# Kernel optimization log

Measured on AMD Instinct MI355X. Metric: run time of the kernel, lower is better.

The kernel has to match this reference:

```python
import jax, jax.numpy as jnp
import numpy as np

D = 256; H = 8; HD = D // H; NK = 32; NLAYERS = 4; FF = 4 * D
B = 8; M = 768; N = 128; LT = 64; T = M + N + LT
SCALE = 1.0 / float(np.sqrt(HD))


def layer_norm(x, s, b):
    mu = x.mean(-1, keepdims=True)
    var = ((x - mu) ** 2).mean(-1, keepdims=True)
    return (x - mu) * jax.lax.rsqrt(var + 1e-5) * s + b


def sine_embed(pos, d):
    # MTR gen_sineembed_for_position: half dims for y, half for x, interleaved sin/cos
    half = d // 2
    dim_t = jnp.power(10000.0, 2.0 * (jnp.arange(half) // 2).astype(jnp.float32) / half)
    scale = 2.0 * np.pi
    def inter(e):
        return jnp.stack([jnp.sin(e[:, 0::2]), jnp.cos(e[:, 1::2])], -1).reshape(e.shape[0], -1)
    ex = pos[:, 0:1] * scale / dim_t
    ey = pos[:, 1:2] * scale / dim_t
    return jnp.concatenate([inter(ey), inter(ex)], -1)


def setup_inputs() -> dict:
    key = jax.random.key(0)
    ks = jax.random.split(key, 24)
    s = 0.02
    inp = {
        'map_token': jax.random.normal(ks[0], (B, M, D), jnp.float32),
        'agent_token': jax.random.normal(ks[1], (B, N, D), jnp.float32),
        'light_token': jax.random.normal(ks[2], (B, LT, D), jnp.float32),
        'map_position': jax.random.uniform(ks[3], (B, M, 2), jnp.float32) * 100.0,
        'agent_position': jax.random.uniform(ks[4], (B, N, 2), jnp.float32) * 100.0,
        'light_position': jax.random.uniform(ks[5], (B, LT, 2), jnp.float32) * 100.0,
        'map_valid_mask': jnp.ones((B, M), bool),
        'agent_valid_mask': jnp.ones((B, N), bool),
        'light_valid_mask': jnp.ones((B, LT), bool),
        'Wq': jax.random.normal(ks[6], (NLAYERS, D, D), jnp.float32) * s,
        'bq': jnp.zeros((NLAYERS, D), jnp.float32),
        'Wk': jax.random.normal(ks[7], (NLAYERS, D, D), jnp.float32) * s,
        'bk': jnp.zeros((NLAYERS, D), jnp.float32),
        'Wv': jax.random.normal(ks[8], (NLAYERS, D, D), jnp.float32) * s,
        'bv': jnp.zeros((NLAYERS, D), jnp.float32),
        'Wo': jax.random.normal(ks[9], (NLAYERS, D, D), jnp.float32) * s,
        'bo': jnp.zeros((NLAYERS, D), jnp.float32),
        'W1': jax.random.normal(ks[10], (NLAYERS, D, FF), jnp.float32) * s,
        'b1': jnp.zeros((NLAYERS, FF), jnp.float32),
        'W2': jax.random.normal(ks[11], (NLAYERS, FF, D), jnp.float32) * s,
        'b2': jnp.zeros((NLAYERS, D), jnp.float32),
        'ln1_s': jnp.ones((NLAYERS, D), jnp.float32),
        'ln1_b': jnp.zeros((NLAYERS, D), jnp.float32),
        'ln2_s': jnp.ones((NLAYERS, D), jnp.float32),
        'ln2_b': jnp.zeros((NLAYERS, D), jnp.float32),
    }
    return inp


def reference(map_token, agent_token, light_token, map_position, agent_position, light_position,
              map_valid_mask, agent_valid_mask, light_valid_mask,
              Wq, bq, Wk, bk, Wv, bv, Wo, bo, W1, b1, W2, b2, ln1_s, ln1_b, ln2_s, ln2_b):
    x = jnp.concatenate([map_token, agent_token, light_token], 1)             # [B,T,D]
    pos = jnp.concatenate([map_position, agent_position, light_position], 1)[..., :2]  # [B,T,2]
    # all tokens valid -> masked compaction is a static reshape
    xs = x.reshape(B * T, D)
    ps = pos.reshape(B * T, 2)
    # KNN within each scene (includes self, like knn_batch_mlogk on same set)
    d2 = jnp.sum((pos[:, :, None, :] - pos[:, None, :, :]) ** 2, -1)          # [B,T,T]
    _, idx = jax.lax.top_k(-d2, NK)                                            # [B,T,NK] local indices
    idx = (idx + (jnp.arange(B) * T)[:, None, None]).reshape(B * T, NK)        # global flat indices
    pe = sine_embed(ps, D)                                                     # [B*T,D]
    out = xs
    for l in range(NLAYERS):
        qk = out + pe
        q = (qk @ Wq[l] + bq[l]).reshape(-1, H, HD)
        k = (qk @ Wk[l] + bk[l]).reshape(-1, H, HD)
        v = (out @ Wv[l] + bv[l]).reshape(-1, H, HD)
        kn = k[idx]                                                            # [BT,NK,H,HD] gather
        vn = v[idx]
        att = jax.nn.softmax(jnp.einsum('nhd,nkhd->nhk', q, kn) * SCALE, axis=-1)
        a = jnp.einsum('nhk,nkhd->nhd', att, vn).reshape(-1, D) @ Wo[l] + bo[l]
        out = layer_norm(out + a, ln1_s[l], ln1_b[l])
        ff = jax.nn.relu(out @ W1[l] + b1[l]) @ W2[l] + b2[l]
        out = layer_norm(out + ff, ln2_s[l], ln2_b[l])
    full = out.reshape(B, T, D)
    return full[:, :M], full[:, M:M + N], full[:, M + N:]
```

## Files before the change

### kernel.cpp

```cpp
#include <hip/hip_runtime.h>
#include <math.h>

#define BB 8
#define MTOK 768
#define NTOK 128
#define LTOK 64
#define TT 960
#define BT 7680
#define DD 256
#define HH 8
#define HD 32
#define KNN 32
#define FFD 1024
#define NLAYERS 4
#define SCALE_ATT 0.17677669529663687f

typedef __attribute__((ext_vector_type(8))) short bfrag_t;
typedef __attribute__((ext_vector_type(4))) float accfrag_t;

__device__ __forceinline__ float b2f(unsigned short u) {
  union { unsigned int i; float f; } c; c.i = ((unsigned int)u) << 16; return c.f;
}
__device__ __forceinline__ unsigned short f2b(float f) {
  union { float f; unsigned int i; } c; c.f = f;
  return (unsigned short)((c.i + 0x7fffu + ((c.i >> 16) & 1u)) >> 16);
}
__device__ __forceinline__ float load_elem(const void* p, size_t i, int f) {
  return f ? b2f(((const unsigned short*)p)[i]) : ((const float*)p)[i];
}
__device__ __forceinline__ size_t pk_addr(int row, int col, int nks) {
  return ((size_t)((row >> 4) * nks + (col >> 5)) << 9)
       + (size_t)(((((col >> 3) & 3) << 4) + (row & 15)) * 8 + (col & 7));
}
__device__ __forceinline__ int swiz_tok(int blk) { return (blk & 7) * TT + (blk >> 3); }

#define FB_BQ 0
#define FB_BK 1024
#define FB_BV 2048
#define FB_BO 3072
#define FB_B1 4096
#define FB_B2 8192
#define FB_LN1S 9216
#define FB_LN1B 10240
#define FB_LN2S 11264
#define FB_LN2B 12288
#define FB_TOTAL 13312
struct ParamSrc { const void* p[13]; };
__global__ __launch_bounds__(256)
void conv_misc_kernel(ParamSrc ps, const void* tok, int* flagout,
                      float* __restrict__ dst, float* __restrict__ posf) {
  __shared__ int cnt;
  if (threadIdx.x == 0) cnt = 0;
  __syncthreads();
  const unsigned short* u = (const unsigned short*)tok;
  int ok = 0;
  for (int i = threadIdx.x; i < 1024; i += 256) {
    int e = (u[i] >> 7) & 0xFF;
    if (e >= 100 && e <= 140) ok++;
  }
  atomicAdd(&cnt, ok);
  __syncthreads();
  int f = (cnt >= 922) ? 1 : 0;
  if (blockIdx.x == 0 && threadIdx.x == 0) *flagout = f;
  if (blockIdx.x < BB) {
    int b = blockIdx.x;
    for (int t = threadIdx.x; t < TT * 2; t += 256) {
      int tok2 = t >> 1, c = t & 1;
      const void* p; size_t idx;
      if (tok2 < MTOK)             { p = ps.p[10]; idx = (size_t)(b * MTOK + tok2) * 2 + c; }
      else if (tok2 < MTOK + NTOK) { p = ps.p[11]; idx = (size_t)(b * NTOK + tok2 - MTOK) * 2 + c; }
      else                         { p = ps.p[12]; idx = (size_t)(b * LTOK + tok2 - MTOK - NTOK) * 2 + c; }
      posf[((size_t)b * TT + tok2) * 2 + c] = load_elem(p, idx, f);
    }
    return;
  }
  int i = (blockIdx.x - BB) * 256 + threadIdx.x;
  if (i >= FB_TOTAL) return;
  int src; size_t off;
  if (i < 4096)      { src = i >> 10;              off = i & 1023; }
  else if (i < 8192) { src = 4;                    off = i - 4096; }
  else               { src = 5 + ((i - 8192) >> 10); off = (i - 8192) & 1023; }
  dst[i] = load_elem(ps.p[src], off, f);
}

__device__ __forceinline__ unsigned long long shfl_xor_u64(unsigned long long v, int m) {
  unsigned lo = (unsigned)v, hi = (unsigned)(v >> 32);
  lo = (unsigned)__shfl_xor((int)lo, m);
  hi = (unsigned)__shfl_xor((int)hi, m);
  return ((unsigned long long)hi << 32) | (unsigned long long)lo;
}
__device__ __forceinline__ unsigned long long shfl_u64(unsigned long long v, int srcLane) {
  unsigned lo = (unsigned)v, hi = (unsigned)(v >> 32);
  lo = (unsigned)__shfl((int)lo, srcLane);
  hi = (unsigned)__shfl((int)hi, srcLane);
  return ((unsigned long long)hi << 32) | (unsigned long long)lo;
}
__device__ __forceinline__ unsigned long long bitonic64(unsigned long long key, int lane) {
#pragma unroll
  for (int kk = 2; kk <= 64; kk <<= 1) {
#pragma unroll
    for (int j = kk >> 1; j > 0; j >>= 1) {
      unsigned long long other = shfl_xor_u64(key, j);
      bool small_ = (lane & j) == 0;
      bool dir = (lane & kk) == 0;
      bool keep = ((key < other) == (small_ == dir));
      key = keep ? key : other;
    }
  }
  return key;
}

struct PackSrc { const void* s[6]; };
__global__ __launch_bounds__(256)
void mega_kernel(PackSrc w, const void* mt, const void* at, const void* lt,
                 const float* __restrict__ posf, const int* __restrict__ flag,
                 unsigned short* __restrict__ Wqkvpk, unsigned short* __restrict__ Wopk,
                 unsigned short* __restrict__ W1pk, unsigned short* __restrict__ W2pk,
                 unsigned short* __restrict__ pe_b, float* __restrict__ out_f,
                 unsigned short* __restrict__ pk1, unsigned short* __restrict__ qkpk,
                 int* __restrict__ idx_out) {
  __shared__ float sx[TT], sy[TT];
  __shared__ unsigned long long cbuf[4][64];
  int bid = blockIdx.x;
  if (bid < 12288) {
    int f = *flag;
    int id = bid * 256 + threadIdx.x;
    if (id < 786432) {
      int layer = id / 196608, rest = id % 196608;
      int sel = rest >> 16, e = rest & 65535;
      int k = e >> 8, col = e & 255;
      const void* src = w.s[sel];
      size_t si = (size_t)layer * 65536 + e;
      Wqkvpk[(size_t)layer * 196608 + (size_t)sel * 65536 + pk_addr(col, k, 8)] =
          f ? ((const unsigned short*)src)[si] : f2b(((const float*)src)[si]);
    } else if (id < 1048576) {
      int off = id - 786432, layer = off >> 16, e = off & 65535;
      int k = e >> 8, col = e & 255;
      size_t si = (size_t)layer * 65536 + e;
      Wopk[(size_t)layer * 65536 + pk_addr(col, k, 8)] =
          f ? ((const unsigned short*)w.s[3])[si] : f2b(((const float*)w.s[3])[si]);
    } else if (id < 2097152) {
      int off = id - 1048576, layer = off >> 18, e = off & 262143;
      int k = e >> 10, col = e & 1023;
      size_t si = (size_t)layer * 262144 + e;
      W1pk[(size_t)layer * 262144 + pk_addr(col, k, 8)] =
          f ? ((const unsigned short*)w.s[4])[si] : f2b(((const float*)w.s[4])[si]);
    } else {
      int off = id - 2097152, layer = off >> 18, e = off & 262143;
      int k = e >> 8, col = e & 255;
      size_t si = (size_t)layer * 262144 + e;
      W2pk[(size_t)layer * 262144 + pk_addr(col, k, 32)] =
          f ? ((const unsigned short*)w.s[5])[si] : f2b(((const float*)w.s[5])[si]);
    }
    return;
  }
  if (bid < 19968) {
    int n = swiz_tok(bid - 12288), d = threadIdx.x;
    int b = n / TT, t = n - b * TT;
    int f = *flag;
    const void* src; size_t si;
    if (t < MTOK)              { src = mt; si = (size_t)(b * MTOK + t) * DD + d; }
    else if (t < MTOK + NTOK)  { src = at; si = (size_t)(b * NTOK + (t - MTOK)) * DD + d; }
    else                       { src = lt; si = (size_t)(b * LTOK + (t - MTOK - NTOK)) * DD + d; }
    float x = load_elem(src, si, f);
    float px = posf[((size_t)b * TT + t) * 2 + 0];
    float py = posf[((size_t)b * TT + t) * 2 + 1];
    float coord = (d < 128) ? py : px;
    int j = d & 127;
    float expo = (float)(2 * (j >> 1)) / 128.0f;
    float dim_t = powf(10000.0f, expo);
    float e = coord * 6.283185307179586f / dim_t;
    float p = (j & 1) ? cosf(e) : sinf(e);
    size_t o = (size_t)n * DD + d;
    pe_b[o] = f2b(p);
    out_f[o] = x;
    size_t pa = pk_addr(n, d, 8);
    pk1[pa] = f2b(x);
    qkpk[pa] = f2b(x + p);
    return;
  }
  int kb = bid - 19968;
  int b = kb & 7;
  int qbase = (kb >> 3) * 4;
  for (int t = threadIdx.x; t < TT; t += 256) {
    sx[t] = posf[((size_t)b * TT + t) * 2 + 0];
    sy[t] = posf[((size_t)b * TT + t) * 2 + 1];
  }
  __syncthreads();
  int wave = threadIdx.x >> 6, lane = threadIdx.x & 63;
  int t = qbase + wave;
  float qx = sx[t], qy = sy[t];

  unsigned long long k[15];
#pragma unroll
  for (int c = 0; c < 15; c++) {
    int j = c * 64 + lane;
    float dx = qx - sx[j], dy = qy - sy[j];
    float d2 = __fadd_rn(__fmul_rn(dx, dx), __fmul_rn(dy, dy));
    k[c] = ((unsigned long long)__float_as_uint(d2) << 32) | (unsigned)j;
  }
  unsigned long long lm = k[0];
#pragma unroll
  for (int c = 1; c < 15; c++) lm = (k[c] < lm) ? k[c] : lm;

  unsigned long long sm = bitonic64(lm, lane);
  unsigned long long thr = shfl_u64(sm, 31);

  int c_l = 0;
#pragma unroll
  for (int c = 0; c < 15; c++) c_l += (k[c] <= thr) ? 1 : 0;
  int inc = c_l;
#pragma unroll
  for (int o = 1; o < 64; o <<= 1) {
    int tt = __shfl_up(inc, o);
    inc += (lane >= o) ? tt : 0;
  }
  int total = __shfl(inc, 63);
  int pos = inc - c_l;

  if (total <= 64) {
    unsigned long long* wb = cbuf[wave];
#pragma unroll
    for (int c = 0; c < 15; c++) {
      if (k[c] <= thr) { wb[pos] = k[c]; pos++; }
    }
    unsigned long long cand = (lane < total) ? wb[lane] : ~0ull;
    cand = bitonic64(cand, lane);
    if (lane < KNN)
      idx_out[((size_t)(b * TT + t)) * KNN + lane] = b * TT + (int)(cand & 0xFFFFFFFFu);
  } else {
    unsigned res = 0;
    for (int i = 0; i < KNN; i++) {
      unsigned long long m = k[0];
#pragma unroll
      for (int c = 1; c < 15; c++) m = (k[c] < m) ? k[c] : m;
#pragma unroll
      for (int o = 32; o > 0; o >>= 1) {
        unsigned long long om = shfl_xor_u64(m, o);
        m = (om < m) ? om : m;
      }
      if (lane == i) res = (unsigned)(m & 0xFFFFFFFFu);
      int owner = (int)(m & 63u), ch = (int)(((unsigned)(m & 0xFFFFFFFFu)) >> 6);
      if (lane == owner) {
#pragma unroll
        for (int c = 0; c < 15; c++) if (c == ch) k[c] = ~0ull;
      }
    }
    if (lane < KNN)
      idx_out[((size_t)(b * TT + t)) * KNN + lane] = b * TT + (int)res;
  }
}

template<int NKS, int NT>
__device__ __forceinline__ void wavegemm(const unsigned short* __restrict__ Apk,
                                         const unsigned short* __restrict__ Bpk,
                                         int rb, int cb0, accfrag_t (&acc)[NT]) {
  const int lane = threadIdx.x & 63;
  accfrag_t z = {0.f, 0.f, 0.f, 0.f};
#pragma unroll
  for (int nt = 0; nt < NT; nt++) acc[nt] = z;
  const unsigned short* ap = Apk + ((size_t)rb * NKS * 512 + lane * 8);
  const unsigned short* bp = Bpk + ((size_t)cb0 * NKS * 512 + lane * 8);
#pragma unroll 4
  for (int ks = 0; ks < NKS; ks++) {
    bfrag_t a = *(const bfrag_t*)(ap + ks * 512);
#pragma unroll
    for (int nt = 0; nt < NT; nt++) {
      bfrag_t b = *(const bfrag_t*)(bp + (size_t)(nt * NKS + ks) * 512);
      acc[nt] = __builtin_amdgcn_mfma_f32_16x16x32_bf16(a, b, acc[nt], 0, 0, 0);
    }
  }
}

__global__ __launch_bounds__(256)
void qkv_kernel(const unsigned short* __restrict__ qkpk,
                const unsigned short* __restrict__ outpk,
                const unsigned short* __restrict__ Wl,
                const float* __restrict__ pb, int l,
                unsigned short* __restrict__ QKV) {
  int scene = blockIdx.x & 7, r = blockIdx.x >> 3;
  int rbg = r % 15, cgall = r / 15;
  int wave = threadIdx.x >> 6, lane = threadIdx.x & 63;
  int rb = scene * 60 + rbg * 4 + wave;
  int sel = cgall >> 2, cg = cgall & 3;
  const unsigned short* A = (sel < 2) ? qkpk : outpk;
  const unsigned short* B = Wl + sel * 65536;
  const float* bias = pb + sel * 1024 + l * 256;
  accfrag_t acc[4];
  wavegemm<8,4>(A, B, rb, cg * 4, acc);
  int l16 = lane & 15, lq = lane >> 4;
  unsigned short* C = QKV + (size_t)sel * BT * DD;
#pragma unroll
  for (int nt = 0; nt < 4; nt++) {
    int col = cg * 64 + nt * 16 + l16;
    float bv = bias[col];
#pragma unroll
    for (int r4 = 0; r4 < 4; r4++) {
      int row = rb * 16 + lq * 4 + r4;
      C[(size_t)row * DD + col] = f2b(acc[nt][r4] + bv);
    }
  }
}

__global__ __launch_bounds__(256)
void attn_kernel(const unsigned short* __restrict__ QKV,
                 const int* __restrict__ idx,
                 unsigned short* __restrict__ attnpk) {
  __shared__ unsigned short kn[KNN][DD + 8];
  __shared__ unsigned short vn[KNN][DD + 8];
  __shared__ float qs[DD];
  __shared__ float att[HH][KNN];
  __shared__ int nb[KNN];
  const unsigned short* Q = QKV;
  const unsigned short* K = QKV + (size_t)BT * DD;
  const unsigned short* V = QKV + 2 * (size_t)BT * DD;
  int n = swiz_tok(blockIdx.x), tid = threadIdx.x;
  if (tid < KNN) nb[tid] = idx[n * KNN + tid];
  qs[tid] = b2f(Q[(size_t)n * DD + tid]);
  __syncthreads();
#pragma unroll
  for (int p = 0; p < 4; p++) {
    int e = p * 256 + tid;
    int r = e >> 5, c8 = (e & 31) * 8;
    int srow = nb[r];
    *(uint4*)(&kn[r][c8]) = *(const uint4*)(K + (size_t)srow * DD + c8);
    *(uint4*)(&vn[r][c8]) = *(const uint4*)(V + (size_t)srow * DD + c8);
  }
  __syncthreads();
  int h = tid >> 5, kk = tid & 31;
  float dot = 0.0f;
#pragma unroll
  for (int d = 0; d < HD; d++) dot += qs[h * HD + d] * b2f(kn[kk][h * HD + d]);
  float sc = dot * SCALE_ATT;
  float mx = sc;
#pragma unroll
  for (int o = 16; o > 0; o >>= 1) mx = fmaxf(mx, __shfl_xor(mx, o, 32));
  float ex = expf(sc - mx);
  float sm = ex;
#pragma unroll
  for (int o = 16; o > 0; o >>= 1) sm += __shfl_xor(sm, o, 32);
  att[h][kk] = ex / sm;
  __syncthreads();
  int d = kk;
  float oacc = 0.0f;
#pragma unroll
  for (int k2 = 0; k2 < KNN; k2++) oacc += att[h][k2] * b2f(vn[k2][h * HD + d]);
  attnpk[pk_addr(n, tid, 8)] = f2b(oacc);
}

template<bool LAST>
__global__ __launch_bounds__(256)
void ffn_block_kernel(const unsigned short* __restrict__ attnpk,
                      const unsigned short* __restrict__ Wo,
                      const unsigned short* __restrict__ W1,
                      const unsigned short* __restrict__ W2,
                      const unsigned short* __restrict__ Wn,
                      const float* __restrict__ bo,
                      const float* __restrict__ b1,
                      const float* __restrict__ b2,
                      const float* __restrict__ pb, int ln,
                      float* __restrict__ yf,
                      const unsigned short* __restrict__ pe_b,
                      const float* __restrict__ g1, const float* __restrict__ t1,
                      const float* __restrict__ g2, const float* __restrict__ t2,
                      unsigned short* __restrict__ QKV,
                      void* __restrict__ dout, const int* __restrict__ flag) {
  __shared__ unsigned short xls[8 * 512];
  __shared__ unsigned short hls[32 * 512];
  __shared__ float ps1[4][16], ps2[4][16];
  int scene = blockIdx.x & 7, rbs = blockIdx.x >> 3;
  int wave = threadIdx.x >> 6, lane = threadIdx.x & 63;
  int rb = scene * 60 + rbs;
  int l16 = lane & 15, lq = lane >> 4;

  float resv[4][4];
#pragma unroll
  for (int nt = 0; nt < 4; nt++) {
    int col = wave * 64 + nt * 16 + l16;
#pragma unroll
    for (int r4 = 0; r4 < 4; r4++) {
      int row = rb * 16 + lq * 4 + r4;
      resv[nt][r4] = yf[(size_t)row * DD + col];
    }
  }

  accfrag_t acc[4];
  wavegemm<8,4>(attnpk, Wo, rb, wave * 4, acc);
  float y[4][4];
  float s[4] = {0.f, 0.f, 0.f, 0.f}, s2[4] = {0.f, 0.f, 0.f, 0.f};
#pragma unroll
  for (int nt = 0; nt < 4; nt++) {
    int col = wave * 64 + nt * 16 + l16;
    float bv = bo[col];
#pragma unroll
    for (int r4 = 0; r4 < 4; r4++) {
      float x = acc[nt][r4] + bv + resv[nt][r4];
      y[nt][r4] = x; s[r4] += x; s2[r4] += x * x;
    }
  }
#pragma unroll
  for (int o = 1; o < 16; o <<= 1) {
#pragma unroll
    for (int r4 = 0; r4 < 4; r4++) { s[r4] += __shfl_xor(s[r4], o); s2[r4] += __shfl_xor(s2[r4], o); }
  }
  if (l16 == 0) {
#pragma unroll
    for (int r4 = 0; r4 < 4; r4++) { ps1[wave][lq * 4 + r4] = s[r4]; ps2[wave][lq * 4 + r4] = s2[r4]; }
  }
  __syncthreads();
#pragma unroll
  for (int r4 = 0; r4 < 4; r4++) {
    int r16 = lq * 4 + r4;
    float ts  = ps1[0][r16] + ps1[1][r16] + ps1[2][r16] + ps1[3][r16];
    float ts2 = ps2[0][r16] + ps2[1][r16] + ps2[2][r16] + ps2[3][r16];
    float mu = ts * (1.0f / 256.0f);
    float var = ts2 * (1.0f / 256.0f) - mu * mu;
    float rstd = 1.0f / sqrtf(fmaxf(var, 0.f) + 1e-5f);
#pragma unroll
    for (int nt = 0; nt < 4; nt++) {
      int col = wave * 64 + nt * 16 + l16;
      float v = (y[nt][r4] - mu) * rstd * g1[col] + t1[col];
      y[nt][r4] = v;
      xls[pk_addr(r16, col, 8)] = f2b(v);
    }
  }
  __syncthreads();

#pragma unroll
  for (int i = 0; i < 4; i++) {
    int cg = wave * 4 + i;
    accfrag_t a2[4];
    wavegemm<8,4>(xls, W1, 0, cg * 4, a2);
#pragma unroll
    for (int nt = 0; nt < 4; nt++) {
      int col = cg * 64 + nt * 16 + l16;
      float bv = b1[col];
#pragma unroll
      for (int r4 = 0; r4 < 4; r4++)
        hls[pk_addr(lq * 4 + r4, col, 32)] = f2b(fmaxf(a2[nt][r4] + bv, 0.0f));
    }
  }
  __syncthreads();

  accfrag_t a3[4];
  wavegemm<32,4>(hls, W2, 0, wave * 4, a3);
  float v2[4][4];
  float s3[4] = {0.f, 0.f, 0.f, 0.f}, s4[4] = {0.f, 0.f, 0.f, 0.f};
#pragma unroll
  for (int nt = 0; nt < 4; nt++) {
    int col = wave * 64 + nt * 16 + l16;
    float bv = b2[col];
#pragma unroll
    for (int r4 = 0; r4 < 4; r4++) {
      float x = a3[nt][r4] + bv + y[nt][r4];
      v2[nt][r4] = x; s3[r4] += x; s4[r4] += x * x;
    }
  }
#pragma unroll
  for (int o = 1; o < 16; o <<= 1) {
#pragma unroll
    for (int r4 = 0; r4 < 4; r4++) { s3[r4] += __shfl_xor(s3[r4], o); s4[r4] += __shfl_xor(s4[r4], o); }
  }
  if (l16 == 0) {
#pragma unroll
    for (int r4 = 0; r4 < 4; r4++) { ps1[wave][lq * 4 + r4] = s3[r4]; ps2[wave][lq * 4 + r4] = s4[r4]; }
  }
  __syncthreads();
  unsigned short* qkls = hls;
  int fl = LAST ? *flag : 0;
#pragma unroll
  for (int r4 = 0; r4 < 4; r4++) {
    int r16 = lq * 4 + r4;
    float ts  = ps1[0][r16] + ps1[1][r16] + ps1[2][r16] + ps1[3][r16];
    float ts2 = ps2[0][r16] + ps2[1][r16] + ps2[2][r16] + ps2[3][r16];
    float mu = ts * (1.0f / 256.0f);
    float var = ts2 * (1.0f / 256.0f) - mu * mu;
    float rstd = 1.0f / sqrtf(fmaxf(var, 0.f) + 1e-5f);
#pragma unroll
    for (int nt = 0; nt < 4; nt++) {
      int col = wave * 64 + nt * 16 + l16;
      float yv = (v2[nt][r4] - mu) * rstd * g2[col] + t2[col];
      int row = rb * 16 + r16;
      if (!LAST) {
        yf[(size_t)row * DD + col] = yv;
        float q = yv + b2f(pe_b[(size_t)row * DD + col]);
        xls[pk_addr(r16, col, 8)] = f2b(yv);
        qkls[pk_addr(r16, col, 8)] = f2b(q);
      } else {
        int t = rbs * 16 + r16;
        size_t o;
        if (t < MTOK)             o = (size_t)(scene * MTOK + t) * DD + col;
        else if (t < MTOK + NTOK) o = (size_t)BB * MTOK * DD + (size_t)(scene * NTOK + (t - MTOK)) * DD + col;
        else                      o = (size_t)BB * MTOK * DD + (size_t)BB * NTOK * DD
                                    + (size_t)(scene * LTOK + (t - MTOK - NTOK)) * DD + col;
        if (fl) ((unsigned short*)dout)[o] = f2b(yv);
        else    ((float*)dout)[o] = yv;
      }
    }
  }

  if (!LAST) {
    __syncthreads();
#pragma unroll
    for (int i = 0; i < 3; i++) {
      int cgall = wave * 3 + i;
      int sel = cgall >> 2, cg = cgall & 3;
      const unsigned short* A = (sel < 2) ? qkls : xls;
      accfrag_t a4[4];
      wavegemm<8,4>(A, Wn + sel * 65536, 0, cg * 4, a4);
      const float* bias = pb + sel * 1024 + ln * 256;
      unsigned short* C = QKV + (size_t)sel * BT * DD;
#pragma unroll
      for (int nt = 0; nt < 4; nt++) {
        int col = cg * 64 + nt * 16 + l16;
        float bv = bias[col];
#pragma unroll
        for (int r4 = 0; r4 < 4; r4++) {
          int row = rb * 16 + lq * 4 + r4;
          C[(size_t)row * DD + col] = f2b(a4[nt][r4] + bv);
        }
      }
    }
  }
}

extern "C" void kernel_launch(void* const* d_in, const int* in_sizes, int n_in,
                              void* d_out, int out_size, void* d_ws, size_t ws_size,
                              hipStream_t stream) {
  const void* map_tok   = d_in[0];
  const void* agent_tok = d_in[1];
  const void* light_tok = d_in[2];
  const void* map_pos   = d_in[3];
  const void* agent_pos = d_in[4];
  const void* light_pos = d_in[5];
  const void* Wq  = d_in[9];
  const void* bq  = d_in[10];
  const void* Wk  = d_in[11];
  const void* bk  = d_in[12];
  const void* Wv  = d_in[13];
  const void* bv  = d_in[14];
  const void* Wo  = d_in[15];
  const void* bo  = d_in[16];
  const void* W1  = d_in[17];
  const void* b1  = d_in[18];
  const void* W2  = d_in[19];
  const void* b2  = d_in[20];
  const void* ln1s = d_in[21];
  const void* ln1b = d_in[22];
  const void* ln2s = d_in[23];
  const void* ln2b = d_in[24];

  size_t off = 0;
  char* base = (char*)d_ws;
  auto take = [&](size_t bytes) { char* p = base + off; off += (bytes + 255) & ~(size_t)255; return (void*)p; };
  int*   flag  = (int*)take(256);
  float* posf  = (float*)take((size_t)BT * 2 * 4);
  float* pbuf  = (float*)take((size_t)FB_TOTAL * 4);
  unsigned short* pe_b = (unsigned short*)take((size_t)BT * DD * 2);
  float* out_f = (float*)take((size_t)BT * DD * 4);
  unsigned short* pk1  = (unsigned short*)take((size_t)BT * DD * 2);
  unsigned short* qkpk = (unsigned short*)take((size_t)BT * DD * 2);
  unsigned short* QKV  = (unsigned short*)take((size_t)3 * BT * DD * 2);
  unsigned short* attnpk = (unsigned short*)take((size_t)BT * DD * 2);
  int* idxb = (int*)take((size_t)BT * KNN * 4);
  unsigned short* Wqkvpk = (unsigned short*)take((size_t)NLAYERS * 3 * DD * DD * 2);
  unsigned short* Wopk   = (unsigned short*)take((size_t)NLAYERS * DD * DD * 2);
  unsigned short* W1pk   = (unsigned short*)take((size_t)NLAYERS * DD * FFD * 2);
  unsigned short* W2pk   = (unsigned short*)take((size_t)NLAYERS * DD * FFD * 2);

  ParamSrc ps; ps.p[0]=bq; ps.p[1]=bk; ps.p[2]=bv; ps.p[3]=bo; ps.p[4]=b1;
  ps.p[5]=b2; ps.p[6]=ln1s; ps.p[7]=ln1b; ps.p[8]=ln2s; ps.p[9]=ln2b;
  ps.p[10]=map_pos; ps.p[11]=agent_pos; ps.p[12]=light_pos;
  conv_misc_kernel<<<BB + (FB_TOTAL + 255) / 256, 256, 0, stream>>>(ps, map_tok, flag, pbuf, posf);

  PackSrc pw; pw.s[0]=Wq; pw.s[1]=Wk; pw.s[2]=Wv; pw.s[3]=Wo; pw.s[4]=W1; pw.s[5]=W2;
  mega_kernel<<<21888, 256, 0, stream>>>(pw, map_tok, agent_tok, light_tok, posf, flag,
                                         Wqkvpk, Wopk, W1pk, W2pk,
                                         pe_b, out_f, pk1, qkpk, idxb);

  qkv_kernel<<<1440, 256, 0, stream>>>(qkpk, pk1, Wqkvpk, pbuf, 0, QKV);

  for (int l = 0; l < NLAYERS; l++) {
    attn_kernel<<<BT, 256, 0, stream>>>(QKV, idxb, attnpk);
    if (l < NLAYERS - 1)
      ffn_block_kernel<false><<<480, 256, 0, stream>>>(
          attnpk, Wopk + (size_t)l * 65536, W1pk + (size_t)l * 262144, W2pk + (size_t)l * 262144,
          Wqkvpk + (size_t)(l + 1) * 196608,
          pbuf + FB_BO + l * 256, pbuf + FB_B1 + l * 1024, pbuf + FB_B2 + l * 256,
          pbuf, l + 1,
          out_f, pe_b,
          pbuf + FB_LN1S + l * 256, pbuf + FB_LN1B + l * 256,
          pbuf + FB_LN2S + l * 256, pbuf + FB_LN2B + l * 256,
          QKV, d_out, flag);
    else
      ffn_block_kernel<true><<<480, 256, 0, stream>>>(
          attnpk, Wopk + (size_t)l * 65536, W1pk + (size_t)l * 262144, W2pk + (size_t)l * 262144,
          Wqkvpk,
          pbuf + FB_BO + l * 256, pbuf + FB_B1 + l * 1024, pbuf + FB_B2 + l * 256,
          pbuf, 0,
          out_f, pe_b,
          pbuf + FB_LN1S + l * 256, pbuf + FB_LN1B + l * 256,
          pbuf + FB_LN2S + l * 256, pbuf + FB_LN2B + l * 256,
          QKV, d_out, flag);
  }
}
```

Measured before the change: 412.0 us.

## Fuse neighbor attention into per-layer FFN kernel with ping-pong QKV buffers

Measured after the change: 423.8 us. +2.9%, slower.

```diff
diff --git a/kernel.cpp b/kernel.cpp
--- a/kernel.cpp
+++ b/kernel.cpp
@@ -302,76 +302,81 @@
   }
 }
 
-__global__ __launch_bounds__(256)
-void attn_kernel(const unsigned short* __restrict__ QKV,
-                 const int* __restrict__ idx,
-                 unsigned short* __restrict__ attnpk) {
-  __shared__ unsigned short kn[KNN][DD + 8];
-  __shared__ unsigned short vn[KNN][DD + 8];
-  __shared__ float qs[DD];
-  __shared__ float att[HH][KNN];
-  __shared__ int nb[KNN];
-  const unsigned short* Q = QKV;
-  const unsigned short* K = QKV + (size_t)BT * DD;
-  const unsigned short* V = QKV + 2 * (size_t)BT * DD;
-  int n = swiz_tok(blockIdx.x), tid = threadIdx.x;
-  if (tid < KNN) nb[tid] = idx[n * KNN + tid];
-  qs[tid] = b2f(Q[(size_t)n * DD + tid]);
-  __syncthreads();
-#pragma unroll
-  for (int p = 0; p < 4; p++) {
-    int e = p * 256 + tid;
-    int r = e >> 5, c8 = (e & 31) * 8;
-    int srow = nb[r];
-    *(uint4*)(&kn[r][c8]) = *(const uint4*)(K + (size_t)srow * DD + c8);
-    *(uint4*)(&vn[r][c8]) = *(const uint4*)(V + (size_t)srow * DD + c8);
-  }
-  __syncthreads();
-  int h = tid >> 5, kk = tid & 31;
-  float dot = 0.0f;
-#pragma unroll
-  for (int d = 0; d < HD; d++) dot += qs[h * HD + d] * b2f(kn[kk][h * HD + d]);
-  float sc = dot * SCALE_ATT;
-  float mx = sc;
-#pragma unroll
-  for (int o = 16; o > 0; o >>= 1) mx = fmaxf(mx, __shfl_xor(mx, o, 32));
-  float ex = expf(sc - mx);
-  float sm = ex;
-#pragma unroll
-  for (int o = 16; o > 0; o >>= 1) sm += __shfl_xor(sm, o, 32);
-  att[h][kk] = ex / sm;
-  __syncthreads();
-  int d = kk;
-  float oacc = 0.0f;
-#pragma unroll
-  for (int k2 = 0; k2 < KNN; k2++) oacc += att[h][k2] * b2f(vn[k2][h * HD + d]);
-  attnpk[pk_addr(n, tid, 8)] = f2b(oacc);
-}
-
 template<bool LAST>
 __global__ __launch_bounds__(256)
-void ffn_block_kernel(const unsigned short* __restrict__ attnpk,
-                      const unsigned short* __restrict__ Wo,
-                      const unsigned short* __restrict__ W1,
-                      const unsigned short* __restrict__ W2,
-                      const unsigned short* __restrict__ Wn,
-                      const float* __restrict__ bo,
-                      const float* __restrict__ b1,
-                      const float* __restrict__ b2,
-                      const float* __restrict__ pb, int ln,
-                      float* __restrict__ yf,
-                      const unsigned short* __restrict__ pe_b,
-                      const float* __restrict__ g1, const float* __restrict__ t1,
-                      const float* __restrict__ g2, const float* __restrict__ t2,
-                      unsigned short* __restrict__ QKV,
-                      void* __restrict__ dout, const int* __restrict__ flag) {
-  __shared__ unsigned short xls[8 * 512];
-  __shared__ unsigned short hls[32 * 512];
+void layer_kernel(const unsigned short* __restrict__ QKVin,
+                  const int* __restrict__ idx,
+                  const unsigned short* __restrict__ Wo,
+                  const unsigned short* __restrict__ W1,
+                  const unsigned short* __restrict__ W2,
+                  const unsigned short* __restrict__ Wn,
+                  const float* __restrict__ bo,
+                  const float* __restrict__ b1,
+                  const float* __restrict__ b2,
+                  const float* __restrict__ pb, int ln,
+                  float* __restrict__ yf,
+                  const unsigned short* __restrict__ pe_b,
+                  const float* __restrict__ g1, const float* __restrict__ t1,
+                  const float* __restrict__ g2, const float* __restrict__ t2,
+                  unsigned short* __restrict__ QKVout,
+                  void* __restrict__ dout, const int* __restrict__ flag) {
+  __shared__ char uA[40960];
+  __shared__ unsigned short apk[4096];
+  __shared__ int nbAll[16][KNN];
   __shared__ float ps1[4][16], ps2[4][16];
+  unsigned short (*kn)[DD + 8] = (unsigned short (*)[DD + 8])uA;
+  unsigned short (*vn)[DD + 8] = (unsigned short (*)[DD + 8])(uA + 16896);
+  float* qs = (float*)(uA + 33792);
+  float (*att)[KNN] = (float (*)[KNN])(uA + 34816);
+  unsigned short* xls = (unsigned short*)uA;
+  unsigned short* hls = (unsigned short*)(uA + 8192);
+
   int scene = blockIdx.x & 7, rbs = blockIdx.x >> 3;
   int wave = threadIdx.x >> 6, lane = threadIdx.x & 63;
   int rb = scene * 60 + rbs;
+  int n0 = rb * 16;
   int l16 = lane & 15, lq = lane >> 4;
+  int tid = threadIdx.x;
+
+  const unsigned short* Qp = QKVin;
+  const unsigned short* Kp = QKVin + (size_t)BT * DD;
+  const unsigned short* Vp = QKVin + 2 * (size_t)BT * DD;
+  for (int i = tid; i < 16 * KNN; i += 256)
+    nbAll[i >> 5][i & 31] = idx[(size_t)(n0 + (i >> 5)) * KNN + (i & 31)];
+  __syncthreads();
+  for (int t16 = 0; t16 < 16; t16++) {
+    int n = n0 + t16;
+    qs[tid] = b2f(Qp[(size_t)n * DD + tid]);
+#pragma unroll
+    for (int p = 0; p < 4; p++) {
+      int e = p * 256 + tid;
+      int r = e >> 5, c8 = (e & 31) * 8;
+      int srow = nbAll[t16][r];
+      *(uint4*)(&kn[r][c8]) = *(const uint4*)(Kp + (size_t)srow * DD + c8);
+      *(uint4*)(&vn[r][c8]) = *(const uint4*)(Vp + (size_t)srow * DD + c8);
+    }
+    __syncthreads();
+    int h = tid >> 5, kk = tid & 31;
+    float dot = 0.0f;
+#pragma unroll
+    for (int d = 0; d < HD; d++) dot += qs[h * HD + d] * b2f(kn[kk][h * HD + d]);
+    float sc = dot * SCALE_ATT;
+    float mx = sc;
+#pragma unroll
+    for (int o = 16; o > 0; o >>= 1) mx = fmaxf(mx, __shfl_xor(mx, o, 32));
+    float ex = expf(sc - mx);
+    float sm = ex;
+#pragma unroll
+    for (int o = 16; o > 0; o >>= 1) sm += __shfl_xor(sm, o, 32);
+    att[h][kk] = ex / sm;
+    __syncthreads();
+    int d = kk;
+    float oacc = 0.0f;
+#pragma unroll
+    for (int k2 = 0; k2 < KNN; k2++) oacc += att[h][k2] * b2f(vn[k2][h * HD + d]);
+    apk[pk_addr(t16, tid, 8)] = f2b(oacc);
+    __syncthreads();
+  }
 
   float resv[4][4];
 #pragma unroll
@@ -385,7 +390,7 @@
   }
 
   accfrag_t acc[4];
-  wavegemm<8,4>(attnpk, Wo, rb, wave * 4, acc);
+  wavegemm<8,4>(apk, Wo, 0, wave * 4, acc);
   float y[4][4];
   float s[4] = {0.f, 0.f, 0.f, 0.f}, s2[4] = {0.f, 0.f, 0.f, 0.f};
 #pragma unroll
@@ -509,7 +514,7 @@
       accfrag_t a4[4];
       wavegemm<8,4>(A, Wn + sel * 65536, 0, cg * 4, a4);
       const float* bias = pb + sel * 1024 + ln * 256;
-      unsigned short* C = QKV + (size_t)sel * BT * DD;
+      unsigned short* C = QKVout + (size_t)sel * BT * DD;
 #pragma unroll
       for (int nt = 0; nt < 4; nt++) {
         int col = cg * 64 + nt * 16 + l16;
@@ -560,8 +565,8 @@
   float* out_f = (float*)take((size_t)BT * DD * 4);
   unsigned short* pk1  = (unsigned short*)take((size_t)BT * DD * 2);
   unsigned short* qkpk = (unsigned short*)take((size_t)BT * DD * 2);
-  unsigned short* QKV  = (unsigned short*)take((size_t)3 * BT * DD * 2);
-  unsigned short* attnpk = (unsigned short*)take((size_t)BT * DD * 2);
+  unsigned short* QKVa = (unsigned short*)take((size_t)3 * BT * DD * 2);
+  unsigned short* QKVb = (unsigned short*)take((size_t)3 * BT * DD * 2);
   int* idxb = (int*)take((size_t)BT * KNN * 4);
   unsigned short* Wqkvpk = (unsigned short*)take((size_t)NLAYERS * 3 * DD * DD * 2);
   unsigned short* Wopk   = (unsigned short*)take((size_t)NLAYERS * DD * DD * 2);
@@ -578,29 +583,32 @@
                                          Wqkvpk, Wopk, W1pk, W2pk,
                                          pe_b, out_f, pk1, qkpk, idxb);
 
-  qkv_kernel<<<1440, 256, 0, stream>>>(qkpk, pk1, Wqkvpk, pbuf, 0, QKV);
+  qkv_kernel<<<1440, 256, 0, stream>>>(qkpk, pk1, Wqkvpk, pbuf, 0, QKVa);
 
   for (int l = 0; l < NLAYERS; l++) {
-    attn_kernel<<<BT, 256, 0, stream>>>(QKV, idxb, attnpk);
+    unsigned short* Qin  = (l & 1) ? QKVb : QKVa;
+    unsigned short* Qout = (l & 1) ? QKVa : QKVb;
     if (l < NLAYERS - 1)
-      ffn_block_kernel<false><<<480, 256, 0, stream>>>(
-          attnpk, Wopk + (size_t)l * 65536, W1pk + (size_t)l * 262144, W2pk + (size_t)l * 262144,
+      layer_kernel<false><<<480, 256, 0, stream>>>(
+          Qin, idxb,
+          Wopk + (size_t)l * 65536, W1pk + (size_t)l * 262144, W2pk + (size_t)l * 262144,
           Wqkvpk + (size_t)(l + 1) * 196608,
           pbuf + FB_BO + l * 256, pbuf + FB_B1 + l * 1024, pbuf + FB_B2 + l * 256,
           pbuf, l + 1,
           out_f, pe_b,
           pbuf + FB_LN1S + l * 256, pbuf + FB_LN1B + l * 256,
           pbuf + FB_LN2S + l * 256, pbuf + FB_LN2B + l * 256,
-          QKV, d_out, flag);
+          Qout, d_out, flag);
     else
-      ffn_block_kernel<true><<<480, 256, 0, stream>>>(
-          attnpk, Wopk + (size_t)l * 65536, W1pk + (size_t)l * 262144, W2pk + (size_t)l * 262144,
+      layer_kernel<true><<<480, 256, 0, stream>>>(
+          Qin, idxb,
+          Wopk + (size_t)l * 65536, W1pk + (size_t)l * 262144, W2pk + (size_t)l * 262144,
           Wqkvpk,
           pbuf + FB_BO + l * 256, pbuf + FB_B1 + l * 1024, pbuf + FB_B2 + l * 256,
           pbuf, 0,
           out_f, pe_b,
           pbuf + FB_LN1S + l * 256, pbuf + FB_LN1B + l * 256,
           pbuf + FB_LN2S + l * 256, pbuf + FB_LN2B + l * 256,
-          QKV, d_out, flag);
-  }
-}
+          Qout, d_out, flag);
+  }
+}
```
